# Kernel tuning notes

Hardware: AMD Instinct MI355X
Metric: run time of the kernel (lower is better)

Reference implementation:

```python
import jax, jax.numpy as jnp
import numpy as np

N_NODES = 100000
N_EDGES = 1600000
N_GRAPHS = 512
IN_F, H1, H2 = 128, 128, 256
N_GROUPS, N_FAM = 16, 10


def setup_inputs() -> dict:
    key = jax.random.key(0)
    ks = jax.random.split(key, 8)
    x = jax.random.normal(ks[0], (N_NODES, IN_F), dtype=jnp.float32)
    edge_index = jax.random.randint(ks[1], (2, N_EDGES), 0, N_NODES, dtype=jnp.int64)
    batch = jnp.sort(jax.random.randint(ks[2], (N_NODES,), 0, N_GRAPHS, dtype=jnp.int64))
    W1 = jax.random.normal(ks[3], (IN_F, H1), dtype=jnp.float32) / np.sqrt(IN_F)
    b1 = jnp.zeros((H1,), dtype=jnp.float32)
    W2 = jax.random.normal(ks[4], (H1, H2), dtype=jnp.float32) / np.sqrt(H1)
    b2 = jnp.zeros((H2,), dtype=jnp.float32)
    Wg = jax.random.normal(ks[5], (H2, N_GROUPS), dtype=jnp.float32) / np.sqrt(H2)
    bg = jnp.zeros((N_GROUPS,), dtype=jnp.float32)
    Wf = jax.random.normal(ks[6], (N_GROUPS, H2, N_FAM), dtype=jnp.float32) / np.sqrt(H2)
    bf = jnp.zeros((N_GROUPS, N_FAM), dtype=jnp.float32)
    return {"x": x, "edge_index": edge_index, "batch": batch,
            "W1": W1, "b1": b1, "W2": W2, "b2": b2,
            "Wg": Wg, "bg": bg, "Wf": Wf, "bf": bf}


def gcn_conv(x, W, b, src, dst, num_nodes):
    # PyG GCNConv: add self-loops, symmetric normalization, scatter-add aggregation.
    xw = x @ W  # [N, out]
    deg = jax.ops.segment_sum(jnp.ones((src.shape[0],), x.dtype), dst,
                              num_segments=num_nodes) + 1.0  # +1 self-loop
    dinv = jax.lax.rsqrt(deg)
    coef = dinv[src] * dinv[dst]            # [E]
    msg = xw[src] * coef[:, None]           # gather + scale (memory-bound)
    agg = jax.ops.segment_sum(msg, dst, num_segments=num_nodes)
    agg = agg + xw * (dinv * dinv)[:, None]  # self-loop contribution
    return agg + b


def reference(x, edge_index, batch, W1, b1, W2, b2, Wg, bg, Wf, bf):
    src, dst = edge_index[0], edge_index[1]
    h = jax.nn.relu(gcn_conv(x, W1, b1, src, dst, N_NODES))
    # dropout p=0.5 is identity in eval mode
    h = gcn_conv(h, W2, b2, src, dst, N_NODES)
    # global mean pool over graphs
    sums = jax.ops.segment_sum(h, batch, num_segments=N_GRAPHS)       # [G, H2]
    cnts = jax.ops.segment_sum(jnp.ones((N_NODES,), h.dtype), batch,
                               num_segments=N_GRAPHS)
    pooled = sums / jnp.maximum(cnts, 1.0)[:, None]
    group_logits = pooled @ Wg + bg                                   # [G, num_groups]
    family_logits = jnp.einsum('bd,gdf->gbf', pooled, Wf) + bf[:, None, :]
    return group_logits, family_logits
```

## Files before the change

### kernel.cpp

```cpp
#include <hip/hip_runtime.h>

#define NN 100000
#define NE 1600000
#define NGR 512
#define KF 128
#define H2F 256
#define NGRP 16
#define NFAM 10

#define CH 128
#define NCHUNK ((NN + CH - 1) / CH)
#define PT 6656
#define NT ((NE + PT - 1) / PT)
#define PREPB_BLKS 64

typedef __attribute__((ext_vector_type(8))) short short8;
typedef __attribute__((ext_vector_type(4))) float floatx4;
typedef __attribute__((ext_vector_type(2))) float floatx2;

__device__ __forceinline__ unsigned short f2bf(float f) {
  unsigned u = __float_as_uint(f);
  unsigned r = (u + 0x7fff + ((u >> 16) & 1)) >> 16;
  return (unsigned short)r;
}
__device__ __forceinline__ float2 bf2f(unsigned u) {
  float2 r;
  r.x = __uint_as_float(u << 16);
  r.y = __uint_as_float(u & 0xffff0000u);
  return r;
}
__device__ __forceinline__ unsigned short pk_fp8(float a, float b) {
  return (unsigned short)__builtin_amdgcn_cvt_pk_fp8_f32(a, b, 0, false);
}
__device__ __forceinline__ floatx2 unpk_fp8(unsigned short u) {
  return __builtin_amdgcn_cvt_pk_f32_fp8((int)u, false);
}


__global__ __launch_bounds__(256) void k_histprep(const int* __restrict__ ei,
                                                  int* __restrict__ tot,
                                                  const float* __restrict__ W,
                                                  unsigned short* __restrict__ Bp) {
  __shared__ int lh[NCHUNK];
  int tid = threadIdx.x;
  if (blockIdx.x >= NT) {
    int idx = (blockIdx.x - NT) * 256 + tid;
    int j = idx & 7;
    int l = (idx >> 3) & 63;
    int rest = idx >> 9;
    int nc = rest & 7;
    int kc = rest >> 3;
    int k = kc * 32 + (l >> 4) * 8 + j;
    int nn = nc * 16 + (l & 15);
    Bp[idx] = f2bf(W[k * KF + nn]);
    return;
  }
  for (int g = tid; g < NCHUNK; g += 256) lh[g] = 0;
  __syncthreads();
  int base = blockIdx.x * PT;
  int nv = min(PT, NE - base);
  for (int i = tid; i < nv; i += 256) atomicAdd(&lh[ei[NE + base + i] >> 7], 1);
  __syncthreads();
  for (int g = tid; g < NCHUNK; g += 256) {
    int v = lh[g];
    if (v) atomicAdd(&tot[g], v);
  }
}


__global__ __launch_bounds__(256) void k_scantot(const int* __restrict__ tot,
                                                 int* __restrict__ cbase,
                                                 int* __restrict__ cursor) {
  __shared__ int ssc[256];
  int tid = threadIdx.x;
  int v4[4]; int loc = 0;
#pragma unroll
  for (int j = 0; j < 4; ++j) {
    int idx = tid * 4 + j;
    v4[j] = (idx < NCHUNK) ? tot[idx] : 0;
    loc += v4[j];
  }
  ssc[tid] = loc;
  __syncthreads();
  for (int off = 1; off < 256; off <<= 1) {
    int val = (tid >= off) ? ssc[tid - off] : 0;
    __syncthreads();
    ssc[tid] += val;
    __syncthreads();
  }
  int excl = ssc[tid] - loc;
#pragma unroll
  for (int j = 0; j < 4; ++j) {
    int idx = tid * 4 + j;
    if (idx < NCHUNK) { cbase[idx] = excl; cursor[idx] = excl; }
    excl += v4[j];
  }
  if (tid == 255) cbase[NCHUNK] = excl;
}


__global__ __launch_bounds__(256) void k_pscatter(const int* __restrict__ ei,
                                                  int* __restrict__ cursor,
                                                  int2* __restrict__ erec) {
  __shared__ int2 stage[PT];
  __shared__ int lstart[NCHUNK];
  __shared__ int lrun[NCHUNK];
  __shared__ int gbase[NCHUNK];
  __shared__ int ssc[256];
  int t0 = blockIdx.x, tid = threadIdx.x;
  for (int g = tid; g < NCHUNK; g += 256) lrun[g] = 0;
  __syncthreads();
  int base = t0 * PT;
  int nv = min(PT, NE - base);
  for (int i = tid; i < nv; i += 256) atomicAdd(&lrun[ei[NE + base + i] >> 7], 1);
  __syncthreads();
  int v4[4]; int loc = 0;
#pragma unroll
  for (int j = 0; j < 4; ++j) {
    int idx = tid * 4 + j;
    v4[j] = (idx < NCHUNK) ? lrun[idx] : 0;
    loc += v4[j];
  }
  ssc[tid] = loc;
  __syncthreads();
  for (int off = 1; off < 256; off <<= 1) {
    int val = (tid >= off) ? ssc[tid - off] : 0;
    __syncthreads();
    ssc[tid] += val;
    __syncthreads();
  }
  int excl = ssc[tid] - loc;
#pragma unroll
  for (int j = 0; j < 4; ++j) {
    int idx = tid * 4 + j;
    if (idx < NCHUNK) lstart[idx] = excl;
    excl += v4[j];
  }
  __syncthreads();
  for (int g = tid; g < NCHUNK; g += 256) {
    int cnt = ((g + 1 < NCHUNK) ? lstart[g + 1] : nv) - lstart[g];
    gbase[g] = cnt ? atomicAdd(&cursor[g], cnt) : 0;
    lrun[g] = lstart[g];
  }
  __syncthreads();
  for (int i = tid; i < nv; i += 256) {
    int s = ei[base + i], d = ei[NE + base + i];
    int pos = atomicAdd(&lrun[d >> 7], 1);
    stage[pos] = make_int2(s, d);
  }
  __syncthreads();
  for (int j = tid; j < nv; j += 256) {
    int2 r = stage[j];
    int g = r.y >> 7;
    erec[gbase[g] + (j - lstart[g])] = r;
  }
}


__global__ __launch_bounds__(256) void k_sort(const int2* __restrict__ erec,
                                              const int* __restrict__ cbase,
                                              int* __restrict__ esrc,
                                              int* __restrict__ rowptr,
                                              float* __restrict__ dinv) {
  __shared__ int hist[CH];
  __shared__ int lrun[CH];
  __shared__ int sc[256];
  const int c = blockIdx.x, tid = threadIdx.x;
  const int e0 = cbase[c], e1 = cbase[c + 1];
  const int nv = e1 - e0;
  if (tid < CH) hist[tid] = 0;
  __syncthreads();
  for (int i = tid; i < nv; i += 256) atomicAdd(&hist[erec[e0 + i].y & (CH - 1)], 1);
  __syncthreads();
  int deg = (tid < CH) ? hist[tid] : 0;
  sc[tid] = deg;
  __syncthreads();
  for (int off = 1; off < 256; off <<= 1) {
    int val = (tid >= off) ? sc[tid - off] : 0;
    __syncthreads();
    sc[tid] += val;
    __syncthreads();
  }
  int excl = sc[tid] - deg;
  int node = c * CH + tid;
  if (tid < CH) {
    lrun[tid] = excl;
    if (node < NN) {
      rowptr[node] = e0 + excl;
      dinv[node] = rsqrtf((float)(deg + 1));
    } else if (node == NN) {
      rowptr[NN] = e0 + excl;
    }
  }
  __syncthreads();
  for (int i = tid; i < nv; i += 256) {
    int2 r = erec[e0 + i];
    int pos = atomicAdd(&lrun[r.y & (CH - 1)], 1);
    esrc[e0 + pos] = r.x;
  }
}


__global__ __launch_bounds__(256) void k_gemm_mfma(const float* __restrict__ A,
                                                   const unsigned short* __restrict__ Bp,
                                                   const float* __restrict__ dinv,
                                                   unsigned short* __restrict__ C) {
  constexpr int K = 128;
  constexpr int NCH = KF / 16;
  const int wv = blockIdx.x * 4 + (threadIdx.x >> 6);
  const int row0 = wv * 16;
  if (row0 >= NN) return;
  const int lane = threadIdx.x & 63;
  const int m = lane & 15;
  const int q = lane >> 4;

  floatx4 acc[NCH];
#pragma unroll
  for (int i = 0; i < NCH; ++i) acc[i] = (floatx4){0.f, 0.f, 0.f, 0.f};

  const int arow = row0 + m;
#pragma unroll
  for (int kc = 0; kc < 4; ++kc) {
    const float* ap = A + (size_t)arow * K + kc * 32 + q * 8;
    float4 f0 = *(const float4*)ap;
    float4 f1 = *(const float4*)(ap + 4);
    short8 af;
    af[0] = (short)f2bf(f0.x); af[1] = (short)f2bf(f0.y);
    af[2] = (short)f2bf(f0.z); af[3] = (short)f2bf(f0.w);
    af[4] = (short)f2bf(f1.x); af[5] = (short)f2bf(f1.y);
    af[6] = (short)f2bf(f1.z); af[7] = (short)f2bf(f1.w);
    const unsigned short* bp = Bp + (size_t)kc * NCH * 512;
#pragma unroll
    for (int nc = 0; nc < NCH; ++nc) {
      short8 bfr = *(const short8*)(bp + (size_t)nc * 512 + lane * 8);
      acc[nc] = __builtin_amdgcn_mfma_f32_16x16x32_bf16(af, bfr, acc[nc], 0, 0, 0);
    }
  }

  float ds[4];
#pragma unroll
  for (int r = 0; r < 4; ++r) ds[r] = dinv[row0 + q * 4 + r];
#pragma unroll
  for (int nc = 0; nc < 4; ++nc) {
#pragma unroll
    for (int r = 0; r < 4; ++r) {
      int row = row0 + q * 4 + r;
      C[(size_t)row * 64 + nc * 16 + m] =
          pk_fp8(acc[nc][r] * ds[r], acc[nc + 4][r] * ds[r]);
    }
  }
}


template <bool FIRST>
__global__ __launch_bounds__(128) void k_agg(const unsigned short* __restrict__ p,
                                             const float* __restrict__ bias,
                                             const int* __restrict__ rowptr,
                                             const int* __restrict__ esrc,
                                             const float* __restrict__ dinv,
                                             void* __restrict__ outp) {
  const int n = blockIdx.x * 2 + (threadIdx.x >> 6);
  const int t = threadIdx.x & 63;
  const int u = t & 31;
  const int half = t >> 5;
  const unsigned* __restrict__ prow = (const unsigned*)p;

  float a0 = 0.f, a1 = 0.f, a2 = 0.f, a3 = 0.f;

  if (half == 0) {
    unsigned v = prow[((unsigned)n << 5) + u];
    floatx2 lo = unpk_fp8((unsigned short)(v & 0xffffu));
    floatx2 hi = unpk_fp8((unsigned short)(v >> 16));
    a0 = lo.x; a1 = lo.y; a2 = hi.x; a3 = hi.y;
  }

  const int r0 = rowptr[n];
  const int r1 = rowptr[n + 1];
  int i = r0;

#define PAIR_TIER(NP)                                                  \
  for (; i + 2 * (NP) <= r1; i += 2 * (NP)) {                          \
    const int ib = i + half;                                           \
    unsigned s[NP];                                                    \
    _Pragma("unroll") for (int j = 0; j < (NP); ++j)                   \
        s[j] = (unsigned)esrc[ib + 2 * j];                             \
    unsigned v[NP];                                                    \
    _Pragma("unroll") for (int j = 0; j < (NP); ++j)                   \
        v[j] = prow[(s[j] << 5) + u];                                  \
    _Pragma("unroll") for (int j = 0; j < (NP); ++j) {                 \
      floatx2 lo = unpk_fp8((unsigned short)(v[j] & 0xffffu));         \
      floatx2 hi = unpk_fp8((unsigned short)(v[j] >> 16));             \
      a0 += lo.x; a1 += lo.y; a2 += hi.x; a3 += hi.y;                  \
    }                                                                  \
  }

  PAIR_TIER(8)
  PAIR_TIER(4)
  PAIR_TIER(2)
  PAIR_TIER(1)
#undef PAIR_TIER

  if (i < r1 && half == 0) {
    unsigned s = (unsigned)esrc[i];
    unsigned v = prow[(s << 5) + u];
    floatx2 lo = unpk_fp8((unsigned short)(v & 0xffffu));
    floatx2 hi = unpk_fp8((unsigned short)(v >> 16));
    a0 += lo.x; a1 += lo.y; a2 += hi.x; a3 += hi.y;
  }

  a0 += __shfl_down(a0, 32, 64);
  a1 += __shfl_down(a1, 32, 64);
  a2 += __shfl_down(a2, 32, 64);
  a3 += __shfl_down(a3, 32, 64);

  if (half == 0) {
    const float dn = dinv[n];
    if (FIRST) {
      float2 blo = *(const float2*)(bias + 2 * u);
      float2 bhi = *(const float2*)(bias + 64 + 2 * u);
      float x0 = fmaxf(fmaf(dn, a0, blo.x), 0.f) * dn;
      float x1 = fmaxf(fmaf(dn, a1, bhi.x), 0.f) * dn;
      float x2 = fmaxf(fmaf(dn, a2, blo.y), 0.f) * dn;
      float x3 = fmaxf(fmaf(dn, a3, bhi.y), 0.f) * dn;
      unsigned lo = pk_fp8(x0, x1);
      unsigned hi = pk_fp8(x2, x3);
      ((unsigned*)outp)[((unsigned)n << 5) + u] = lo | (hi << 16);
    } else {
      float x0 = a0 * dn, x1 = a1 * dn, x2 = a2 * dn, x3 = a3 * dn;
      uint2 w;
      w.x = (unsigned)f2bf(x0) | ((unsigned)f2bf(x1) << 16);
      w.y = (unsigned)f2bf(x2) | ((unsigned)f2bf(x3) << 16);
      ((uint2*)outp)[((unsigned)n << 5) + u] = w;
    }
  }
}


__global__ __launch_bounds__(256) void k_poolheads(const unsigned* __restrict__ hp,
                                                   const int* __restrict__ batch,
                                                   const float* __restrict__ W2,
                                                   const float* __restrict__ b2,
                                                   const float* __restrict__ Wg,
                                                   const float* __restrict__ bg,
                                                   const float* __restrict__ Wf,
                                                   const float* __restrict__ bfb,
                                                   float* __restrict__ out) {
  __shared__ float sh[4][128];
  __shared__ float pr[KF];
  __shared__ float p[H2F];
  __shared__ int bnd[2];
  const int g = blockIdx.x;
  const int tid = threadIdx.x;
  if (tid < 2) {
    int target = g + tid;
    int lo = 0, hi = NN;
    while (lo < hi) { int mid = (lo + hi) >> 1; if (batch[mid] < target) lo = mid + 1; else hi = mid; }
    bnd[tid] = lo;
  }
  __syncthreads();
  const int start = bnd[0], end = bnd[1];
  const int t = tid & 63, wv = tid >> 6;

  float sx = 0.f, sy = 0.f;
  int n = start + wv;
  for (; n + 12 < end; n += 16) {
    unsigned u0 = hp[(size_t)n * 64 + t];
    unsigned u1 = hp[(size_t)(n + 4) * 64 + t];
    unsigned u2 = hp[(size_t)(n + 8) * 64 + t];
    unsigned u3 = hp[(size_t)(n + 12) * 64 + t];
    float2 f0 = bf2f(u0), f1 = bf2f(u1), f2 = bf2f(u2), f3 = bf2f(u3);
    sx += (f0.x + f1.x) + (f2.x + f3.x);
    sy += (f0.y + f1.y) + (f2.y + f3.y);
  }
  for (; n < end; n += 4) {
    float2 f = bf2f(hp[(size_t)n * 64 + t]);
    sx += f.x; sy += f.y;
  }
  sh[wv][2 * t] = sx;
  sh[wv][2 * t + 1] = sy;
  __syncthreads();
  if (wv == 0) {
    float vx = sh[0][2 * t] + sh[1][2 * t] + sh[2][2 * t] + sh[3][2 * t];
    float vy = sh[0][2 * t + 1] + sh[1][2 * t + 1] + sh[2][2 * t + 1] + sh[3][2 * t + 1];
    float c = fmaxf((float)(end - start), 1.f);
    pr[t] = vx / c;
    pr[t + 64] = vy / c;
  }
  __syncthreads();
  float acc = b2[tid];
#pragma unroll 8
  for (int d = 0; d < KF; ++d) acc = fmaf(pr[d], W2[d * H2F + tid], acc);
  p[tid] = acc;
  __syncthreads();
  if (tid < NGRP) {
    float a = bg[tid];
    for (int d = 0; d < H2F; ++d) a = fmaf(p[d], Wg[d * NGRP + tid], a);
    out[g * NGRP + tid] = a;
  } else if (tid >= 64 && tid < 64 + NGRP * NFAM) {
    int u = tid - 64;
    int gg = u / NFAM;
    int ff = u % NFAM;
    float a = bfb[gg * NFAM + ff];
    for (int d = 0; d < H2F; ++d) a = fmaf(p[d], Wf[(gg * H2F + d) * NFAM + ff], a);
    out[NGR * NGRP + (size_t)gg * NGR * NFAM + g * NFAM + ff] = a;
  }
}


extern "C" void kernel_launch(void* const* d_in, const int* in_sizes, int n_in,
                              void* d_out, int out_size, void* d_ws, size_t ws_size,
                              hipStream_t stream) {
  const float* x    = (const float*)d_in[0];
  const int*   ei   = (const int*)d_in[1];
  const int*   batch= (const int*)d_in[2];
  const float* W1   = (const float*)d_in[3];
  const float* b1   = (const float*)d_in[4];
  const float* W2   = (const float*)d_in[5];
  const float* b2   = (const float*)d_in[6];
  const float* Wg   = (const float*)d_in[7];
  const float* bg   = (const float*)d_in[8];
  const float* Wf   = (const float*)d_in[9];
  const float* bfb  = (const float*)d_in[10];
  float* out = (float*)d_out;

  char* w = (char*)d_ws;
  auto take = [&](size_t bytes) {
    char* p = w;
    w += (bytes + 255) & ~(size_t)255;
    return (void*)p;
  };
  int*   tot   = (int*)take((size_t)NCHUNK * 4);
  int*   cbase = (int*)take((size_t)(NCHUNK + 1) * 4);
  int*   cursor= (int*)take((size_t)NCHUNK * 4);
  int2*  erec  = (int2*)take((size_t)NE * 8);
  int*   esrc  = (int*)take((size_t)NE * 4);
  int*   rowptr= (int*)take((size_t)(NN + 1) * 4);
  float* dinv  = (float*)take((size_t)NN * 4);
  unsigned short* Bp1 = (unsigned short*)take((size_t)KF * KF * 2);
  unsigned short* xw1 = (unsigned short*)take((size_t)NN * 64 * 2);
  unsigned short* h1  = (unsigned short*)take((size_t)NN * 64 * 2);
  unsigned* agg2= (unsigned*)take((size_t)NN * KF * 2);

  hipMemsetAsync(tot, 0, (size_t)NCHUNK * 4, stream);
  k_histprep<<<NT + PREPB_BLKS, 256, 0, stream>>>(ei, tot, W1, Bp1);
  k_scantot<<<1, 256, 0, stream>>>(tot, cbase, cursor);
  k_pscatter<<<NT, 256, 0, stream>>>(ei, cursor, erec);
  k_sort<<<NCHUNK, 256, 0, stream>>>(erec, cbase, esrc, rowptr, dinv);

  k_gemm_mfma<<<1563, 256, 0, stream>>>(x, Bp1, dinv, xw1);

  k_agg<true><<<NN / 2, 128, 0, stream>>>(xw1, b1, rowptr, esrc, dinv, h1);
  k_agg<false><<<NN / 2, 128, 0, stream>>>(h1, nullptr, rowptr, esrc, dinv, agg2);

  k_poolheads<<<NGR, 256, 0, stream>>>(agg2, batch, W2, b2, Wg, bg, Wf, bfb, out);
}
```

Baseline: 299.5 us.

## Fuse second GCN aggregation with mean pooling via per-edge destination weights

```diff
diff --git a/kernel.cpp b/kernel.cpp
--- a/kernel.cpp
+++ b/kernel.cpp
@@ -17,6 +17,7 @@
 typedef __attribute__((ext_vector_type(8))) short short8;
 typedef __attribute__((ext_vector_type(4))) float floatx4;
 typedef __attribute__((ext_vector_type(2))) float floatx2;
+typedef __attribute__((ext_vector_type(2))) unsigned uintx2;
 
 __device__ __forceinline__ unsigned short f2bf(float f) {
   unsigned u = __float_as_uint(f);
@@ -160,10 +161,12 @@
 __global__ __launch_bounds__(256) void k_sort(const int2* __restrict__ erec,
                                               const int* __restrict__ cbase,
                                               int* __restrict__ esrc,
+                                              float* __restrict__ ew,
                                               int* __restrict__ rowptr,
                                               float* __restrict__ dinv) {
   __shared__ int hist[CH];
   __shared__ int lrun[CH];
+  __shared__ float ldv[CH];
   __shared__ int sc[256];
   const int c = blockIdx.x, tid = threadIdx.x;
   const int e0 = cbase[c], e1 = cbase[c + 1];
@@ -186,8 +189,10 @@
   if (tid < CH) {
     lrun[tid] = excl;
     if (node < NN) {
+      float dv = rsqrtf((float)(deg + 1));
       rowptr[node] = e0 + excl;
-      dinv[node] = rsqrtf((float)(deg + 1));
+      dinv[node] = dv;
+      ldv[tid] = dv;
     } else if (node == NN) {
       rowptr[NN] = e0 + excl;
     }
@@ -195,8 +200,10 @@
   __syncthreads();
   for (int i = tid; i < nv; i += 256) {
     int2 r = erec[e0 + i];
-    int pos = atomicAdd(&lrun[r.y & (CH - 1)], 1);
+    int ln = r.y & (CH - 1);
+    int pos = atomicAdd(&lrun[ln], 1);
     esrc[e0 + pos] = r.x;
+    ew[e0 + pos] = ldv[ln];
   }
 }
 
@@ -252,13 +259,12 @@
 }
 
 
-template <bool FIRST>
-__global__ __launch_bounds__(128) void k_agg(const unsigned short* __restrict__ p,
-                                             const float* __restrict__ bias,
-                                             const int* __restrict__ rowptr,
-                                             const int* __restrict__ esrc,
-                                             const float* __restrict__ dinv,
-                                             void* __restrict__ outp) {
+__global__ __launch_bounds__(128) void k_agg1(const unsigned short* __restrict__ p,
+                                              const float* __restrict__ bias,
+                                              const int* __restrict__ rowptr,
+                                              const int* __restrict__ esrc,
+                                              const float* __restrict__ dinv,
+                                              unsigned short* __restrict__ outp) {
   const int n = blockIdx.x * 2 + (threadIdx.x >> 6);
   const int t = threadIdx.x & 63;
   const int u = t & 31;
@@ -315,39 +321,35 @@
 
   if (half == 0) {
     const float dn = dinv[n];
-    if (FIRST) {
-      float2 blo = *(const float2*)(bias + 2 * u);
-      float2 bhi = *(const float2*)(bias + 64 + 2 * u);
-      float x0 = fmaxf(fmaf(dn, a0, blo.x), 0.f) * dn;
-      float x1 = fmaxf(fmaf(dn, a1, bhi.x), 0.f) * dn;
-      float x2 = fmaxf(fmaf(dn, a2, blo.y), 0.f) * dn;
-      float x3 = fmaxf(fmaf(dn, a3, bhi.y), 0.f) * dn;
-      unsigned lo = pk_fp8(x0, x1);
-      unsigned hi = pk_fp8(x2, x3);
-      ((unsigned*)outp)[((unsigned)n << 5) + u] = lo | (hi << 16);
-    } else {
-      float x0 = a0 * dn, x1 = a1 * dn, x2 = a2 * dn, x3 = a3 * dn;
-      uint2 w;
-      w.x = (unsigned)f2bf(x0) | ((unsigned)f2bf(x1) << 16);
-      w.y = (unsigned)f2bf(x2) | ((unsigned)f2bf(x3) << 16);
-      ((uint2*)outp)[((unsigned)n << 5) + u] = w;
-    }
-  }
-}
-
-
-__global__ __launch_bounds__(256) void k_poolheads(const unsigned* __restrict__ hp,
-                                                   const int* __restrict__ batch,
-                                                   const float* __restrict__ W2,
-                                                   const float* __restrict__ b2,
-                                                   const float* __restrict__ Wg,
-                                                   const float* __restrict__ bg,
-                                                   const float* __restrict__ Wf,
-                                                   const float* __restrict__ bfb,
-                                                   float* __restrict__ out) {
-  __shared__ float sh[4][128];
+    float2 blo = *(const float2*)(bias + 2 * u);
+    float2 bhi = *(const float2*)(bias + 64 + 2 * u);
+    float x0 = fmaxf(fmaf(dn, a0, blo.x), 0.f) * dn;
+    float x1 = fmaxf(fmaf(dn, a1, bhi.x), 0.f) * dn;
+    float x2 = fmaxf(fmaf(dn, a2, blo.y), 0.f) * dn;
+    float x3 = fmaxf(fmaf(dn, a3, bhi.y), 0.f) * dn;
+    unsigned lo = pk_fp8(x0, x1);
+    unsigned hi = pk_fp8(x2, x3);
+    ((unsigned*)outp)[((unsigned)n << 5) + u] = lo | (hi << 16);
+  }
+}
+
+
+__global__ __launch_bounds__(512) void k_aggpool(const unsigned short* __restrict__ p,
+                                                 const int* __restrict__ batch,
+                                                 const int* __restrict__ rowptr,
+                                                 const int* __restrict__ esrc,
+                                                 const float* __restrict__ ew,
+                                                 const float* __restrict__ dinv,
+                                                 const float* __restrict__ W2,
+                                                 const float* __restrict__ b2,
+                                                 const float* __restrict__ Wg,
+                                                 const float* __restrict__ bg,
+                                                 const float* __restrict__ Wf,
+                                                 const float* __restrict__ bfb,
+                                                 float* __restrict__ out) {
+  __shared__ float sacc[8][128];
   __shared__ float pr[KF];
-  __shared__ float p[H2F];
+  __shared__ float pp[H2F];
   __shared__ int bnd[2];
   const int g = blockIdx.x;
   const int tid = threadIdx.x;
@@ -359,49 +361,93 @@
   }
   __syncthreads();
   const int start = bnd[0], end = bnd[1];
-  const int t = tid & 63, wv = tid >> 6;
-
-  float sx = 0.f, sy = 0.f;
-  int n = start + wv;
-  for (; n + 12 < end; n += 16) {
-    unsigned u0 = hp[(size_t)n * 64 + t];
-    unsigned u1 = hp[(size_t)(n + 4) * 64 + t];
-    unsigned u2 = hp[(size_t)(n + 8) * 64 + t];
-    unsigned u3 = hp[(size_t)(n + 12) * 64 + t];
-    float2 f0 = bf2f(u0), f1 = bf2f(u1), f2 = bf2f(u2), f3 = bf2f(u3);
-    sx += (f0.x + f1.x) + (f2.x + f3.x);
-    sy += (f0.y + f1.y) + (f2.y + f3.y);
-  }
-  for (; n < end; n += 4) {
-    float2 f = bf2f(hp[(size_t)n * 64 + t]);
-    sx += f.x; sy += f.y;
-  }
-  sh[wv][2 * t] = sx;
-  sh[wv][2 * t + 1] = sy;
-  __syncthreads();
-  if (wv == 0) {
-    float vx = sh[0][2 * t] + sh[1][2 * t] + sh[2][2 * t] + sh[3][2 * t];
-    float vy = sh[0][2 * t + 1] + sh[1][2 * t + 1] + sh[2][2 * t + 1] + sh[3][2 * t + 1];
+  const int wv = tid >> 6, t = tid & 63, u = t & 31, half = t >> 5;
+  const unsigned* __restrict__ prow = (const unsigned*)p;
+
+  float a0 = 0.f, a1 = 0.f, a2 = 0.f, a3 = 0.f;
+
+  const int e0 = rowptr[start];
+  const int e1 = rowptr[end];
+
+#define EDGE_STEP(idx)                                                 \
+  {                                                                    \
+    unsigned s_ = (unsigned)esrc[(idx)];                               \
+    float w_ = ew[(idx)];                                              \
+    unsigned v_ = prow[(s_ << 5) + u];                                 \
+    floatx2 lo = unpk_fp8((unsigned short)(v_ & 0xffffu));             \
+    floatx2 hi = unpk_fp8((unsigned short)(v_ >> 16));                 \
+    a0 = fmaf(w_, lo.x, a0); a1 = fmaf(w_, lo.y, a1);                  \
+    a2 = fmaf(w_, hi.x, a2); a3 = fmaf(w_, hi.y, a3);                  \
+  }
+
+  int i = e0 + wv * 2 + half;
+  for (; i + 48 < e1; i += 64) {
+    int i0 = i, i1 = i + 16, i2 = i + 32, i3 = i + 48;
+    unsigned s0 = (unsigned)esrc[i0], s1 = (unsigned)esrc[i1];
+    unsigned s2 = (unsigned)esrc[i2], s3 = (unsigned)esrc[i3];
+    float w0 = ew[i0], w1 = ew[i1], w2 = ew[i2], w3 = ew[i3];
+    unsigned v0 = prow[(s0 << 5) + u];
+    unsigned v1 = prow[(s1 << 5) + u];
+    unsigned v2 = prow[(s2 << 5) + u];
+    unsigned v3 = prow[(s3 << 5) + u];
+    floatx2 f;
+    f = unpk_fp8((unsigned short)(v0 & 0xffffu)); a0 = fmaf(w0, f.x, a0); a1 = fmaf(w0, f.y, a1);
+    f = unpk_fp8((unsigned short)(v0 >> 16));     a2 = fmaf(w0, f.x, a2); a3 = fmaf(w0, f.y, a3);
+    f = unpk_fp8((unsigned short)(v1 & 0xffffu)); a0 = fmaf(w1, f.x, a0); a1 = fmaf(w1, f.y, a1);
+    f = unpk_fp8((unsigned short)(v1 >> 16));     a2 = fmaf(w1, f.x, a2); a3 = fmaf(w1, f.y, a3);
+    f = unpk_fp8((unsigned short)(v2 & 0xffffu)); a0 = fmaf(w2, f.x, a0); a1 = fmaf(w2, f.y, a1);
+    f = unpk_fp8((unsigned short)(v2 >> 16));     a2 = fmaf(w2, f.x, a2); a3 = fmaf(w2, f.y, a3);
+    f = unpk_fp8((unsigned short)(v3 & 0xffffu)); a0 = fmaf(w3, f.x, a0); a1 = fmaf(w3, f.y, a1);
+    f = unpk_fp8((unsigned short)(v3 >> 16));     a2 = fmaf(w3, f.x, a2); a3 = fmaf(w3, f.y, a3);
+  }
+  for (; i < e1; i += 16) EDGE_STEP(i)
+#undef EDGE_STEP
+
+  for (int n = start + wv * 2 + half; n < end; n += 16) {
+    float w_ = dinv[n];
+    unsigned v_ = prow[((unsigned)n << 5) + u];
+    floatx2 lo = unpk_fp8((unsigned short)(v_ & 0xffffu));
+    floatx2 hi = unpk_fp8((unsigned short)(v_ >> 16));
+    a0 = fmaf(w_, lo.x, a0); a1 = fmaf(w_, lo.y, a1);
+    a2 = fmaf(w_, hi.x, a2); a3 = fmaf(w_, hi.y, a3);
+  }
+
+  a0 += __shfl_down(a0, 32, 64);
+  a1 += __shfl_down(a1, 32, 64);
+  a2 += __shfl_down(a2, 32, 64);
+  a3 += __shfl_down(a3, 32, 64);
+  if (half == 0) {
+    sacc[wv][2 * u] = a0;
+    sacc[wv][2 * u + 1] = a2;
+    sacc[wv][2 * u + 64] = a1;
+    sacc[wv][2 * u + 65] = a3;
+  }
+  __syncthreads();
+  if (tid < KF) {
+    float v = 0.f;
+#pragma unroll
+    for (int w = 0; w < 8; ++w) v += sacc[w][tid];
     float c = fmaxf((float)(end - start), 1.f);
-    pr[t] = vx / c;
-    pr[t + 64] = vy / c;
-  }
-  __syncthreads();
-  float acc = b2[tid];
+    pr[tid] = v / c;
+  }
+  __syncthreads();
+  if (tid < H2F) {
+    float acc = b2[tid];
 #pragma unroll 8
-  for (int d = 0; d < KF; ++d) acc = fmaf(pr[d], W2[d * H2F + tid], acc);
-  p[tid] = acc;
+    for (int d = 0; d < KF; ++d) acc = fmaf(pr[d], W2[d * H2F + tid], acc);
+    pp[tid] = acc;
+  }
   __syncthreads();
   if (tid < NGRP) {
     float a = bg[tid];
-    for (int d = 0; d < H2F; ++d) a = fmaf(p[d], Wg[d * NGRP + tid], a);
+    for (int d = 0; d < H2F; ++d) a = fmaf(pp[d], Wg[d * NGRP + tid], a);
     out[g * NGRP + tid] = a;
   } else if (tid >= 64 && tid < 64 + NGRP * NFAM) {
-    int u = tid - 64;
-    int gg = u / NFAM;
-    int ff = u % NFAM;
+    int uu = tid - 64;
+    int gg = uu / NFAM;
+    int ff = uu % NFAM;
     float a = bfb[gg * NFAM + ff];
-    for (int d = 0; d < H2F; ++d) a = fmaf(p[d], Wf[(gg * H2F + d) * NFAM + ff], a);
+    for (int d = 0; d < H2F; ++d) a = fmaf(pp[d], Wf[(gg * H2F + d) * NFAM + ff], a);
     out[NGR * NGRP + (size_t)gg * NGR * NFAM + g * NFAM + ff] = a;
   }
 }
@@ -434,23 +480,22 @@
   int*   cursor= (int*)take((size_t)NCHUNK * 4);
   int2*  erec  = (int2*)take((size_t)NE * 8);
   int*   esrc  = (int*)take((size_t)NE * 4);
+  float* ew    = (float*)take((size_t)NE * 4);
   int*   rowptr= (int*)take((size_t)(NN + 1) * 4);
   float* dinv  = (float*)take((size_t)NN * 4);
   unsigned short* Bp1 = (unsigned short*)take((size_t)KF * KF * 2);
   unsigned short* xw1 = (unsigned short*)take((size_t)NN * 64 * 2);
   unsigned short* h1  = (unsigned short*)take((size_t)NN * 64 * 2);
-  unsigned* agg2= (unsigned*)take((size_t)NN * KF * 2);
 
   hipMemsetAsync(tot, 0, (size_t)NCHUNK * 4, stream);
   k_histprep<<<NT + PREPB_BLKS, 256, 0, stream>>>(ei, tot, W1, Bp1);
   k_scantot<<<1, 256, 0, stream>>>(tot, cbase, cursor);
   k_pscatter<<<NT, 256, 0, stream>>>(ei, cursor, erec);
-  k_sort<<<NCHUNK, 256, 0, stream>>>(erec, cbase, esrc, rowptr, dinv);
+  k_sort<<<NCHUNK, 256, 0, stream>>>(erec, cbase, esrc, ew, rowptr, dinv);
 
   k_gemm_mfma<<<1563, 256, 0, stream>>>(x, Bp1, dinv, xw1);
 
-  k_agg<true><<<NN / 2, 128, 0, stream>>>(xw1, b1, rowptr, esrc, dinv, h1);
-  k_agg<false><<<NN / 2, 128, 0, stream>>>(h1, nullptr, rowptr, esrc, dinv, agg2);
-
-  k_poolheads<<<NGR, 256, 0, stream>>>(agg2, batch, W2, b2, Wg, bg, Wf, bfb, out);
-}
+  k_agg1<<<NN / 2, 128, 0, stream>>>(xw1, b1, rowptr, esrc, dinv, h1);
+  k_aggpool<<<NGR, 512, 0, stream>>>(h1, batch, rowptr, esrc, ew, dinv,
+                                     W2, b2, Wg, bg, Wf, bfb, out);
+}
```

Measured after the change: 301.1 us. Within noise of the previous version (+0.5%).
